# Kernel optimization log

Measured on AMD Instinct MI355X. Metric: run time of the kernel, lower is better.

## Reference

```python
import jax, jax.numpy as jnp
import numpy as np

N_HEADS = 16
D_MODEL = 1024
D_HEAD = D_MODEL // N_HEADS


def setup_inputs() -> dict:
    key = jax.random.key(0)
    k1, k2, k3 = jax.random.split(key, 3)
    b, t, d = 2, 2048, D_MODEL
    x = jax.random.normal(k1, (b, t, d), dtype=jnp.float32)
    # Linear weights stored as [in, out] so y = x @ W (equivalent to torch's x @ W.T)
    w_qkv = jax.random.normal(k2, (d, 3 * d), dtype=jnp.float32) * (1.0 / np.sqrt(d))
    w_out = jax.random.normal(k3, (d, d), dtype=jnp.float32) * (1.0 / np.sqrt(d))
    return {"x": x, "w_qkv": w_qkv, "w_out": w_out}


def reference(x, w_qkv, w_out):
    b, t, d = x.shape
    h, dh = N_HEADS, D_HEAD
    qkv = x @ w_qkv                                   # (b, t, 3d)
    q, k, v = jnp.split(qkv, 3, axis=-1)
    # (b, h, t, dh)
    q = q.reshape(b, t, h, dh).transpose(0, 2, 1, 3)
    k = k.reshape(b, t, h, dh).transpose(0, 2, 1, 3)
    v = v.reshape(b, t, h, dh).transpose(0, 2, 1, 3)
    scale = 1.0 / np.sqrt(dh).astype(np.float32)
    att = jnp.einsum('bhqd,bhkd->bhqk', q, k) * scale  # (b, h, t, t)
    causal = jnp.tril(jnp.ones((t, t), dtype=bool))
    att = jnp.where(causal, att, -jnp.inf)
    att = jax.nn.softmax(att, axis=-1)
    y = jnp.einsum('bhqk,bhkd->bhqd', att, v)          # (b, h, t, dh)
    y = y.transpose(0, 2, 1, 3).reshape(b, t, d)
    return y @ w_out
```

## Files before the change

### kernel.cpp

```cpp
#include <hip/hip_runtime.h>
#include <hip/hip_bf16.h>
#include <stdint.h>

typedef __bf16 bf16x8 __attribute__((ext_vector_type(8)));
typedef float  f32x4  __attribute__((ext_vector_type(4)));

#define B_   2
#define T_   2048
#define H_   16
#define DH_  64
#define DM_  1024
#define BH_  (B_*H_)
#define M_   (B_*T_)

#define QSCALE 0.18033688f
#define FIXED_M 8.0f

static __device__ __forceinline__ void gload_lds16(const void* g, void* lds) {
  __builtin_amdgcn_global_load_lds(
      (const __attribute__((address_space(1))) void*)(uintptr_t)g,
      (__attribute__((address_space(3))) void*)(uint32_t)(uintptr_t)lds,
      16, 0, 0);
}

__global__ void k_cvt_bf16(const float* __restrict__ in, __hip_bfloat16* __restrict__ out, int n4) {
  int i = blockIdx.x * blockDim.x + threadIdx.x;
  if (i < n4) {
    float4 v = reinterpret_cast<const float4*>(in)[i];
    alignas(8) __hip_bfloat16 t[4] = {__float2bfloat16(v.x), __float2bfloat16(v.y),
                                      __float2bfloat16(v.z), __float2bfloat16(v.w)};
    reinterpret_cast<uint2*>(out)[i] = *reinterpret_cast<const uint2*>(t);
  }
}

__global__ void k_cvtT(const float* __restrict__ in, __hip_bfloat16* __restrict__ out, int K, int N) {
  __shared__ float tile[32][33];
  int n0 = blockIdx.x * 32, k0 = blockIdx.y * 32;
  int tid = threadIdx.x;
  int kl = tid >> 3, n4 = (tid & 7) * 4;
  float4 v = *reinterpret_cast<const float4*>(in + (size_t)(k0 + kl) * N + n0 + n4);
  tile[kl][n4 + 0] = v.x; tile[kl][n4 + 1] = v.y; tile[kl][n4 + 2] = v.z; tile[kl][n4 + 3] = v.w;
  __syncthreads();
  int nl = tid >> 3, k4 = (tid & 7) * 4;
  alignas(8) __hip_bfloat16 t[4];
  #pragma unroll
  for (int j = 0; j < 4; ++j) t[j] = __float2bfloat16(tile[k4 + j][nl]);
  *reinterpret_cast<uint2*>(out + (size_t)(n0 + nl) * K + k0 + k4) = *reinterpret_cast<const uint2*>(t);
}

template<int BM, int BN, int FM, int FN>
static __device__ __forceinline__ void gemm_core(
    const __hip_bfloat16* __restrict__ A, const __hip_bfloat16* __restrict__ BT,
    int K, int brow, int bcol, __hip_bfloat16* As, __hip_bfloat16* Bs, f32x4 acc[FM][FN]) {
  constexpr int WGN = BN / (16 * FN);
  const int tid = threadIdx.x, wave = tid >> 6, lane = tid & 63;
  const int wr = wave / WGN, wc = wave % WGN;
  const int llo = lane & 15, lhi = lane >> 4;
  for (int k0 = 0; k0 < K; k0 += 32) {
    #pragma unroll
    for (int c = wave; c < BM / 16; c += 4)
      gload_lds16(A + (size_t)(brow + c * 16 + (lane >> 2)) * K + k0 + (lane & 3) * 8,
                  As + c * 16 * 32);
    #pragma unroll
    for (int c = wave; c < BN / 16; c += 4)
      gload_lds16(BT + (size_t)(bcol + c * 16 + (lane >> 2)) * K + k0 + (lane & 3) * 8,
                  Bs + c * 16 * 32);
    __syncthreads();
    bf16x8 a[FM], b[FN];
    #pragma unroll
    for (int i = 0; i < FM; ++i)
      a[i] = *reinterpret_cast<const bf16x8*>(As + (wr * FM * 16 + i * 16 + llo) * 32 + lhi * 8);
    #pragma unroll
    for (int j = 0; j < FN; ++j)
      b[j] = *reinterpret_cast<const bf16x8*>(Bs + (wc * FN * 16 + j * 16 + llo) * 32 + lhi * 8);
    #pragma unroll
    for (int i = 0; i < FM; ++i)
      #pragma unroll
      for (int j = 0; j < FN; ++j)
        acc[i][j] = __builtin_amdgcn_mfma_f32_16x16x32_bf16(a[i], b[j], acc[i][j], 0, 0, 0);
    __syncthreads();
  }
}

__global__ __launch_bounds__(256) void k_gemm_qkv(
    const __hip_bfloat16* __restrict__ A, const __hip_bfloat16* __restrict__ BT,
    __hip_bfloat16* __restrict__ q_ws, __hip_bfloat16* __restrict__ k_ws,
    __hip_bfloat16* __restrict__ vT) {
  alignas(16) __shared__ __hip_bfloat16 As[128 * 32];
  alignas(16) __shared__ __hip_bfloat16 Bs[128 * 32];
  f32x4 acc[4][4] = {};
  const int brow = blockIdx.y * 128, bcol = blockIdx.x * 128;
  gemm_core<128, 128, 4, 4>(A, BT, DM_, brow, bcol, As, Bs, acc);
  const int tid = threadIdx.x, wave = tid >> 6, lane = tid & 63;
  const int wr = wave >> 1, wc = wave & 1;
  const int llo = lane & 15, lhi = lane >> 4;
  #pragma unroll
  for (int i = 0; i < 4; ++i) {
    const int tbase = brow + wr * 64 + i * 16 + lhi * 4;
    const int b = tbase >> 11, t = tbase & 2047;
    #pragma unroll
    for (int j = 0; j < 4; ++j) {
      int n = bcol + wc * 64 + j * 16 + llo;
      int part = n >> 10, rem = n & 1023, hh = rem >> 6, dh = rem & 63;
      if (part == 2) {
        alignas(8) __hip_bfloat16 tv[4];
        #pragma unroll
        for (int r = 0; r < 4; ++r) tv[r] = __float2bfloat16(acc[i][j][r]);
        *reinterpret_cast<uint2*>(
            vT + (((size_t)(b * H_ + hh)) * DH_ + dh) * T_ + t) =
            *reinterpret_cast<const uint2*>(tv);
      } else {
        float sc = (part == 0) ? QSCALE : 1.0f;
        __hip_bfloat16* dst = (part == 0) ? q_ws : k_ws;
        #pragma unroll
        for (int r = 0; r < 4; ++r)
          dst[(((size_t)(b * H_ + hh)) * T_ + t + r) * DH_ + dh] =
              __float2bfloat16(acc[i][j][r] * sc);
      }
    }
  }
}

__global__ __launch_bounds__(256) void k_gemm_out(
    const __hip_bfloat16* __restrict__ A, const __hip_bfloat16* __restrict__ BT,
    float* __restrict__ C) {
  alignas(16) __shared__ __hip_bfloat16 As[128 * 32];
  alignas(16) __shared__ __hip_bfloat16 Bs[64 * 32];
  f32x4 acc[4][2] = {};
  const int brow = blockIdx.y * 128, bcol = blockIdx.x * 64;
  gemm_core<128, 64, 4, 2>(A, BT, DM_, brow, bcol, As, Bs, acc);
  const int tid = threadIdx.x, wave = tid >> 6, lane = tid & 63;
  const int wr = wave >> 1, wc = wave & 1;
  const int llo = lane & 15, lhi = lane >> 4;
  #pragma unroll
  for (int i = 0; i < 4; ++i)
    #pragma unroll
    for (int j = 0; j < 2; ++j) {
      int n = bcol + wc * 32 + j * 16 + llo;
      #pragma unroll
      for (int r = 0; r < 4; ++r) {
        int m = brow + wr * 64 + i * 16 + lhi * 4 + r;
        C[(size_t)m * DM_ + n] = acc[i][j][r];
      }
    }
}

__global__ __launch_bounds__(512) void k_attn(
    const __hip_bfloat16* __restrict__ Q, const __hip_bfloat16* __restrict__ Kk,
    const __hip_bfloat16* __restrict__ VT, __hip_bfloat16* __restrict__ Y) {
  alignas(16) __shared__ __hip_bfloat16 Ks[4][64 * 64];
  alignas(16) __shared__ __hip_bfloat16 Vs[4][64 * 64];
  alignas(16) __shared__ __hip_bfloat16 Ps[8][16 * 64];
  const int bh = blockIdx.y;
  const int p  = blockIdx.x;
  const int tid = threadIdx.x, wave = tid >> 6, lane = tid & 63;
  const int llo = lane & 15, lhi = lane >> 4;
  const int qt   = (wave < 4) ? (31 - p) : p;
  const int myNt = qt + 1;
  const int ntA  = 32 - p;
  const int q0 = qt * 64;
  const int qbase = q0 + (wave & 3) * 16;

  const __hip_bfloat16* kb = Kk + (size_t)bh * T_ * DH_;
  const __hip_bfloat16* vb = VT + (size_t)bh * DH_ * T_;

  const int srow = lane >> 3;
  const int schunk = (lane & 7) ^ srow;
  const int rb = wave * 8;

  bf16x8 aq[2];
  #pragma unroll
  for (int k0 = 0; k0 < 2; ++k0)
    aq[k0] = *reinterpret_cast<const bf16x8*>(
        Q + ((size_t)bh * T_ + qbase + llo) * DH_ + k0 * 32 + lhi * 8);

  float lrow[4] = {0.f, 0.f, 0.f, 0.f};
  f32x4 o[4] = {};

  gload_lds16(kb + (size_t)(rb + srow) * DH_ + schunk * 8, &Ks[0][rb * 64]);
  gload_lds16(vb + (size_t)(rb + srow) * T_ + schunk * 8, &Vs[0][rb * 64]);
  gload_lds16(kb + (size_t)(64 + rb + srow) * DH_ + schunk * 8, &Ks[1][rb * 64]);
  gload_lds16(vb + (size_t)(rb + srow) * T_ + 64 + schunk * 8, &Vs[1][rb * 64]);

  for (int it = 0; it < ntA; ++it) {
    const int cur = it & 3;
    {
      const int ts = (it + 2 < ntA) ? (it + 2) : (ntA - 1);
      const int bs = (it + 2) & 3;
      const int tn = ts * 64;
      gload_lds16(kb + (size_t)(tn + rb + srow) * DH_ + schunk * 8, &Ks[bs][rb * 64]);
      gload_lds16(vb + (size_t)(rb + srow) * T_ + tn + schunk * 8, &Vs[bs][rb * 64]);
    }
    asm volatile("s_waitcnt vmcnt(4)" ::: "memory");
    __builtin_amdgcn_sched_barrier(0);
    __builtin_amdgcn_s_barrier();
    __builtin_amdgcn_sched_barrier(0);

    if (it < myNt) {
      const __hip_bfloat16* ksb = Ks[cur];
      const __hip_bfloat16* vsb = Vs[cur];

      f32x4 s[4];
      __builtin_amdgcn_s_setprio(1);
      #pragma unroll
      for (int jn = 0; jn < 4; ++jn) {
        const __hip_bfloat16* krow = ksb + (jn * 16 + llo) * 64;
        bf16x8 b0 = *reinterpret_cast<const bf16x8*>(krow + ((lhi ^ (llo & 7)) << 3));
        bf16x8 b1 = *reinterpret_cast<const bf16x8*>(krow + (((4 + lhi) ^ (llo & 7)) << 3));
        f32x4 z = {};
        z = __builtin_amdgcn_mfma_f32_16x16x32_bf16(aq[0], b0, z, 0, 0, 0);
        z = __builtin_amdgcn_mfma_f32_16x16x32_bf16(aq[1], b1, z, 0, 0, 0);
        s[jn] = z;
      }
      __builtin_amdgcn_s_setprio(0);
      if (it == myNt - 1) {
        #pragma unroll
        for (int jn = 0; jn < 4; ++jn)
          #pragma unroll
          for (int r = 0; r < 4; ++r) {
            int qrow = qbase + lhi * 4 + r;
            int tcol = q0 + jn * 16 + llo;
            if (tcol > qrow) s[jn][r] = -INFINITY;
          }
      }
      #pragma unroll
      for (int jn = 0; jn < 4; ++jn)
        #pragma unroll
        for (int r = 0; r < 4; ++r) {
          float pv = __builtin_amdgcn_exp2f(s[jn][r] - FIXED_M);
          lrow[r] += pv;
          int row = lhi * 4 + r, col = jn * 16 + llo;
          Ps[wave][row * 64 + (col ^ ((row & 7) << 3))] = __float2bfloat16(pv);
        }
      bf16x8 ap0 = *reinterpret_cast<const bf16x8*>(
          &Ps[wave][llo * 64 + ((lhi ^ (llo & 7)) << 3)]);
      bf16x8 ap1 = *reinterpret_cast<const bf16x8*>(
          &Ps[wave][llo * 64 + (((4 + lhi) ^ (llo & 7)) << 3)]);
      __builtin_amdgcn_s_setprio(1);
      #pragma unroll
      for (int jd = 0; jd < 4; ++jd) {
        const __hip_bfloat16* vrow = vsb + (jd * 16 + llo) * 64;
        bf16x8 b0 = *reinterpret_cast<const bf16x8*>(vrow + ((lhi ^ (llo & 7)) << 3));
        bf16x8 b1 = *reinterpret_cast<const bf16x8*>(vrow + (((4 + lhi) ^ (llo & 7)) << 3));
        o[jd] = __builtin_amdgcn_mfma_f32_16x16x32_bf16(ap0, b0, o[jd], 0, 0, 0);
        o[jd] = __builtin_amdgcn_mfma_f32_16x16x32_bf16(ap1, b1, o[jd], 0, 0, 0);
      }
      __builtin_amdgcn_s_setprio(0);
    }
  }

  float lr[4];
  #pragma unroll
  for (int r = 0; r < 4; ++r) {
    float ps = lrow[r];
    #pragma unroll
    for (int d = 1; d < 16; d <<= 1) ps += __shfl_xor(ps, d);
    lr[r] = ps;
  }
  const int b = bh >> 4, h = bh & 15;
  #pragma unroll
  for (int jd = 0; jd < 4; ++jd)
    #pragma unroll
    for (int r = 0; r < 4; ++r) {
      int trow = qbase + lhi * 4 + r;
      int col = h * 64 + jd * 16 + llo;
      Y[((size_t)(b * T_ + trow)) * DM_ + col] = __float2bfloat16(o[jd][r] / lr[r]);
    }
}

extern "C" void kernel_launch(void* const* d_in, const int* in_sizes, int n_in,
                              void* d_out, int out_size, void* d_ws, size_t ws_size,
                              hipStream_t stream) {
  const float* x     = (const float*)d_in[0];
  const float* w_qkv = (const float*)d_in[1];
  const float* w_out = (const float*)d_in[2];
  float* out = (float*)d_out;
  char* ws = (char*)d_ws;

  size_t off = 0;
  __hip_bfloat16* xb    = (__hip_bfloat16*)(ws + off); off += (size_t)M_ * DM_ * 2;
  __hip_bfloat16* wqkvT = (__hip_bfloat16*)(ws + off); off += (size_t)3 * DM_ * DM_ * 2;
  __hip_bfloat16* woutT = (__hip_bfloat16*)(ws + off); off += (size_t)DM_ * DM_ * 2;
  __hip_bfloat16* q_ws  = (__hip_bfloat16*)(ws + off); off += (size_t)M_ * DM_ * 2;
  __hip_bfloat16* k_ws  = (__hip_bfloat16*)(ws + off); off += (size_t)M_ * DM_ * 2;
  __hip_bfloat16* vT    = (__hip_bfloat16*)(ws + off); off += (size_t)M_ * DM_ * 2;
  __hip_bfloat16* y_ws  = (__hip_bfloat16*)(ws + off); off += (size_t)M_ * DM_ * 2;
  (void)ws_size; (void)in_sizes; (void)n_in; (void)out_size;

  k_cvt_bf16<<<(M_ * DM_ / 4 + 255) / 256, 256, 0, stream>>>(x, xb, M_ * DM_ / 4);
  k_cvtT<<<dim3(3 * DM_ / 32, DM_ / 32), 256, 0, stream>>>(w_qkv, wqkvT, DM_, 3 * DM_);
  k_cvtT<<<dim3(DM_ / 32, DM_ / 32), 256, 0, stream>>>(w_out, woutT, DM_, DM_);

  k_gemm_qkv<<<dim3(3 * DM_ / 128, M_ / 128), 256, 0, stream>>>(xb, wqkvT, q_ws, k_ws, vT);

  k_attn<<<dim3(T_ / 128, BH_), 512, 0, stream>>>(q_ws, k_ws, vT, y_ws);

  k_gemm_out<<<dim3(DM_ / 64, M_ / 128), 256, 0, stream>>>(y_ws, woutT, out);
}
```

Baseline: 112.2 us.

## Triple-buffer GEMM LDS tiles with async global-to-LDS prefetch two stages ahead

Replaces the single-buffered GEMM main loop, which synced twice per k-step, with a three-slot LDS ring. Loads for step k+2 are issued right after one barrier, and explicit vmcnt waits make only the oldest stage complete before compute. Wave priority is also raised around the MFMA block. This should hide global load latency in both the QKV and output projections, at the cost of tripling LDS use per block, which may lower occupancy.

```diff
diff --git a/kernel.cpp b/kernel.cpp
--- a/kernel.cpp
+++ b/kernel.cpp
@@ -49,48 +49,67 @@
 }
 
 template<int BM, int BN, int FM, int FN>
-static __device__ __forceinline__ void gemm_core(
+static __device__ __forceinline__ void gemm_core_pipe(
     const __hip_bfloat16* __restrict__ A, const __hip_bfloat16* __restrict__ BT,
-    int K, int brow, int bcol, __hip_bfloat16* As, __hip_bfloat16* Bs, f32x4 acc[FM][FN]) {
+    int K, int brow, int bcol, __hip_bfloat16* As, __hip_bfloat16* Bs,
+    f32x4 acc[FM][FN]) {
   constexpr int WGN = BN / (16 * FN);
+  constexpr int LOADS = BM / 64 + BN / 64;
+  constexpr int ASLOT = BM * 32, BSLOT = BN * 32;
   const int tid = threadIdx.x, wave = tid >> 6, lane = tid & 63;
   const int wr = wave / WGN, wc = wave % WGN;
   const int llo = lane & 15, lhi = lane >> 4;
-  for (int k0 = 0; k0 < K; k0 += 32) {
+  const int nk = K / 32;
+  auto stage = [&](int ks, int slot) {
     #pragma unroll
     for (int c = wave; c < BM / 16; c += 4)
-      gload_lds16(A + (size_t)(brow + c * 16 + (lane >> 2)) * K + k0 + (lane & 3) * 8,
-                  As + c * 16 * 32);
+      gload_lds16(A + (size_t)(brow + c * 16 + (lane >> 2)) * K + ks * 32 + (lane & 3) * 8,
+                  As + slot * ASLOT + c * 512);
     #pragma unroll
     for (int c = wave; c < BN / 16; c += 4)
-      gload_lds16(BT + (size_t)(bcol + c * 16 + (lane >> 2)) * K + k0 + (lane & 3) * 8,
-                  Bs + c * 16 * 32);
-    __syncthreads();
+      gload_lds16(BT + (size_t)(bcol + c * 16 + (lane >> 2)) * K + ks * 32 + (lane & 3) * 8,
+                  Bs + slot * BSLOT + c * 512);
+  };
+  stage(0, 0);
+  stage(1, 1);
+  for (int ks = 0; ks < nk; ++ks) {
+    if constexpr (LOADS == 4)      asm volatile("s_waitcnt vmcnt(4)" ::: "memory");
+    else if constexpr (LOADS == 3) asm volatile("s_waitcnt vmcnt(3)" ::: "memory");
+    else                           asm volatile("s_waitcnt vmcnt(0)" ::: "memory");
+    __builtin_amdgcn_sched_barrier(0);
+    __builtin_amdgcn_s_barrier();
+    __builtin_amdgcn_sched_barrier(0);
+    const int s2 = (ks + 2 < nk) ? ks + 2 : nk - 1;
+    stage(s2, (ks + 2) % 3);
+    const __hip_bfloat16* Asl = As + (ks % 3) * ASLOT;
+    const __hip_bfloat16* Bsl = Bs + (ks % 3) * BSLOT;
     bf16x8 a[FM], b[FN];
     #pragma unroll
     for (int i = 0; i < FM; ++i)
-      a[i] = *reinterpret_cast<const bf16x8*>(As + (wr * FM * 16 + i * 16 + llo) * 32 + lhi * 8);
+      a[i] = *reinterpret_cast<const bf16x8*>(Asl + (wr * FM * 16 + i * 16 + llo) * 32 + lhi * 8);
     #pragma unroll
     for (int j = 0; j < FN; ++j)
-      b[j] = *reinterpret_cast<const bf16x8*>(Bs + (wc * FN * 16 + j * 16 + llo) * 32 + lhi * 8);
+      b[j] = *reinterpret_cast<const bf16x8*>(Bsl + (wc * FN * 16 + j * 16 + llo) * 32 + lhi * 8);
+    __builtin_amdgcn_s_setprio(1);
     #pragma unroll
     for (int i = 0; i < FM; ++i)
       #pragma unroll
       for (int j = 0; j < FN; ++j)
         acc[i][j] = __builtin_amdgcn_mfma_f32_16x16x32_bf16(a[i], b[j], acc[i][j], 0, 0, 0);
-    __syncthreads();
-  }
+    __builtin_amdgcn_s_setprio(0);
+  }
+  asm volatile("s_waitcnt vmcnt(0)" ::: "memory");
 }
 
 __global__ __launch_bounds__(256) void k_gemm_qkv(
     const __hip_bfloat16* __restrict__ A, const __hip_bfloat16* __restrict__ BT,
     __hip_bfloat16* __restrict__ q_ws, __hip_bfloat16* __restrict__ k_ws,
     __hip_bfloat16* __restrict__ vT) {
-  alignas(16) __shared__ __hip_bfloat16 As[128 * 32];
-  alignas(16) __shared__ __hip_bfloat16 Bs[128 * 32];
+  alignas(16) __shared__ __hip_bfloat16 As[3 * 128 * 32];
+  alignas(16) __shared__ __hip_bfloat16 Bs[3 * 128 * 32];
   f32x4 acc[4][4] = {};
   const int brow = blockIdx.y * 128, bcol = blockIdx.x * 128;
-  gemm_core<128, 128, 4, 4>(A, BT, DM_, brow, bcol, As, Bs, acc);
+  gemm_core_pipe<128, 128, 4, 4>(A, BT, DM_, brow, bcol, As, Bs, acc);
   const int tid = threadIdx.x, wave = tid >> 6, lane = tid & 63;
   const int wr = wave >> 1, wc = wave & 1;
   const int llo = lane & 15, lhi = lane >> 4;
@@ -124,11 +143,11 @@
 __global__ __launch_bounds__(256) void k_gemm_out(
     const __hip_bfloat16* __restrict__ A, const __hip_bfloat16* __restrict__ BT,
     float* __restrict__ C) {
-  alignas(16) __shared__ __hip_bfloat16 As[128 * 32];
-  alignas(16) __shared__ __hip_bfloat16 Bs[64 * 32];
+  alignas(16) __shared__ __hip_bfloat16 As[3 * 128 * 32];
+  alignas(16) __shared__ __hip_bfloat16 Bs[3 * 64 * 32];
   f32x4 acc[4][2] = {};
   const int brow = blockIdx.y * 128, bcol = blockIdx.x * 64;
-  gemm_core<128, 64, 4, 2>(A, BT, DM_, brow, bcol, As, Bs, acc);
+  gemm_core_pipe<128, 64, 4, 2>(A, BT, DM_, brow, bcol, As, Bs, acc);
   const int tid = threadIdx.x, wave = tid >> 6, lane = tid & 63;
   const int wr = wave >> 1, wc = wave & 1;
   const int llo = lane & 15, lhi = lane >> 4;
```

Result: faster. 106.1 us (-5.5%).
